# Optimization experiments

Measured on AMD Instinct MI355X. Metric: run time of the kernel, lower is better.

Reference implementation:

```python
import jax, jax.numpy as jnp
import numpy as np
import math

B, T, C = 4, 2048, 2048
N_HEAD, N_KV = 16, 4
HD = C // N_HEAD          # 128
N_REP = N_HEAD // N_KV    # 4


def setup_inputs() -> dict:
    key = jax.random.key(0)
    ks = jax.random.split(key, 5)
    x = jax.random.normal(ks[0], (B, T, C), dtype=jnp.float32)
    s = 0.02
    wq = jax.random.normal(ks[1], (C, N_HEAD * HD), dtype=jnp.float32) * s
    wk = jax.random.normal(ks[2], (C, N_KV * HD), dtype=jnp.float32) * s
    wv = jax.random.normal(ks[3], (C, N_KV * HD), dtype=jnp.float32) * s
    wo = jax.random.normal(ks[4], (C, C), dtype=jnp.float32) * s
    # RoPE table: cos/sin pairs, equivalent to torch polar freqs_cis (theta=10000)
    inv_freq = 1.0 / (10000.0 ** (jnp.arange(0, HD, 2, dtype=jnp.float32) / HD))  # (HD/2,)
    ang = jnp.arange(T, dtype=jnp.float32)[:, None] * inv_freq[None, :]           # (T, HD/2)
    freqs_cis = jnp.stack([jnp.cos(ang), jnp.sin(ang)], axis=-1)                  # (T, HD/2, 2)
    return {"x": x, "freqs_cis": freqs_cis, "wq": wq, "wk": wk, "wv": wv, "wo": wo}


def _rope(t, freqs_cis):
    # t: (B, T, H, HD); complex multiply on (even, odd) pairs
    tp = t.reshape(*t.shape[:-1], HD // 2, 2)
    a, b = tp[..., 0], tp[..., 1]
    c = freqs_cis[: t.shape[1], :, 0][None, :, None, :]  # (1,T,1,HD/2)
    s = freqs_cis[: t.shape[1], :, 1][None, :, None, :]
    out = jnp.stack([a * c - b * s, a * s + b * c], axis=-1)
    return out.reshape(t.shape).astype(t.dtype)


def reference(x, freqs_cis, wq, wk, wv, wo):
    q = (x @ wq).reshape(B, T, N_HEAD, HD)
    k = (x @ wk).reshape(B, T, N_KV, HD)
    v = (x @ wv).reshape(B, T, N_KV, HD)
    q = _rope(q, freqs_cis)
    k = _rope(k, freqs_cis)
    # GQA attention without materializing repeated K/V: group q heads by kv head
    qg = q.reshape(B, T, N_KV, N_REP, HD)
    scale = 1.0 / math.sqrt(HD)
    att = jnp.einsum('btgrd,bsgd->bgrts', qg, k) * scale   # (B,G,R,T,S)
    causal = jnp.tril(jnp.ones((T, T), dtype=bool))
    att = jnp.where(causal, att, jnp.finfo(att.dtype).min)
    att = jax.nn.softmax(att, axis=-1)
    y = jnp.einsum('bgrts,bsgd->btgrd', att, v).reshape(B, T, C)
    y = y @ wo
    return y
```

## Files before the change

### kernel.cpp

```cpp
#include <hip/hip_runtime.h>
#include <math.h>
#include <stdint.h>

#define B_ 4
#define T_ 2048
#define C_ 2048
#define NH 16
#define NKV 4
#define HD 128
#define NREP 4
#define KVC (NKV*HD)
#define QSTR 3072

typedef __attribute__((ext_vector_type(8))) __bf16 bf16x8;
typedef __attribute__((ext_vector_type(4))) __bf16 bf16x4;
typedef __attribute__((ext_vector_type(4))) float floatx4;

#define GLOBAL_AS __attribute__((address_space(1)))
#define LDS_AS __attribute__((address_space(3)))

__device__ __forceinline__ void gl2lds16(const unsigned short* g, unsigned short* l) {
  __builtin_amdgcn_global_load_lds((const GLOBAL_AS unsigned int*)g,
                                   (LDS_AS unsigned int*)l, 16, 0, 0);
}

__device__ __forceinline__ float b2f(unsigned short u) {
  union { unsigned int i; float f; } v; v.i = ((unsigned int)u) << 16; return v.f;
}
__device__ __forceinline__ unsigned short f2b(float f) {
  union { float f; unsigned int i; } v; v.f = f;
  unsigned int r = v.i + 0x7fffu + ((v.i >> 16) & 1u);
  return (unsigned short)(r >> 16);
}

__global__ void cvt_bf16_kernel(const float* __restrict__ X,
                                unsigned short* __restrict__ Y, int n) {
  int i = (blockIdx.x * 256 + threadIdx.x) * 4;
  if (i >= n) return;
  float4 v = *(const float4*)(X + i);
  ushort4 o;
  o.x = f2b(v.x); o.y = f2b(v.y); o.z = f2b(v.z); o.w = f2b(v.w);
  *(ushort4*)(Y + i) = o;
}

__global__ void transpose_cvt_kernel(const float* __restrict__ W,
                                     unsigned short* __restrict__ Wt,
                                     int K, int N) {
  __shared__ float tile[32][33];
  int n = blockIdx.x * 32 + threadIdx.x;
  int kbase = blockIdx.y * 32;
  #pragma unroll
  for (int i = 0; i < 32; i += 8)
    tile[threadIdx.y + i][threadIdx.x] = W[(size_t)(kbase + threadIdx.y + i) * N + n];
  __syncthreads();
  int k = kbase + threadIdx.x;
  int nb = blockIdx.x * 32;
  #pragma unroll
  for (int i = 0; i < 32; i += 8)
    Wt[(size_t)(nb + threadIdx.y + i) * K + k] = f2b(tile[threadIdx.x][threadIdx.y + i]);
}

__global__ void transpose_v_kernel(const unsigned short* __restrict__ V,
                                   unsigned short* __restrict__ Vt) {
  __shared__ unsigned short tile[32][33];
  int d0 = blockIdx.x * 32;
  int sg = blockIdx.y * 32;
  int b = sg >> 11;
  int s0 = sg & (T_ - 1);
  #pragma unroll
  for (int i = 0; i < 32; i += 8)
    tile[threadIdx.y + i][threadIdx.x] =
        V[(size_t)(sg + threadIdx.y + i) * QSTR + d0 + threadIdx.x];
  __syncthreads();
  #pragma unroll
  for (int i = 0; i < 32; i += 8) {
    int d = d0 + threadIdx.y + i;
    int g = d >> 7, dl = d & 127;
    Vt[((size_t)(b * NKV + g) * HD + dl) * T_ + s0 + threadIdx.x] =
        tile[threadIdx.x][threadIdx.y + i];
  }
}

template<int STORE_BF16>
__global__ __launch_bounds__(512, 2) void gemm256_bt(
    const unsigned short* __restrict__ A,
    const unsigned short* __restrict__ Bt,
    void* __restrict__ Cout,
    int M, int N, int K)
{
  __shared__ unsigned short Lds[65536];

  int tid = threadIdx.x;

  int nbx = gridDim.x;
  int nwg = nbx * gridDim.y;
  int orig = blockIdx.y * nbx + blockIdx.x;
  int cpx = nwg >> 3;
  int swz = (orig & 7) * cpx + (orig >> 3);
  int m0 = (swz % nbx) * 256;
  int n0 = (swz / nbx) * 256;

  int wave = tid >> 6, lane = tid & 63;
  int fr = lane & 15, kg = lane >> 4;
  int slot = kg ^ ((fr >> 1) & 3);
  int wm_off = (wave >> 2) * 128;
  int wn_off = (wave & 3) * 64;

  int rowoff = wave * 16 + (lane >> 2);
  int kgs = (lane & 3) ^ ((lane >> 3) & 3);
  const unsigned short* Asrc = A  + (size_t)(m0 + rowoff) * K + kgs * 8;
  const unsigned short* Bsrc = Bt + (size_t)(n0 + rowoff) * K + kgs * 8;
  size_t rstep = (size_t)128 * K;

  int abase = (wm_off + fr) * 32 + slot * 8;
  int bbase = 8192 + (wn_off + fr) * 32 + slot * 8;

  floatx4 acc[8][4];
  #pragma unroll
  for (int i = 0; i < 8; i++)
    #pragma unroll
    for (int j = 0; j < 4; j++)
      acc[i][j] = (floatx4){0.f, 0.f, 0.f, 0.f};

  int nt = K >> 6;

  #define STAGE_HALF(tn, kkh, isB) do {                                        \
    const unsigned short* s_ = ((isB) ? Bsrc : Asrc) + (size_t)(tn) * 64 + (kkh) * 32; \
    unsigned short* d_ = &Lds[(((tn) & 1) << 15) + ((kkh) << 14) + ((isB) << 13) + (wave << 9)]; \
    gl2lds16(s_, d_);                                                          \
    gl2lds16(s_ + rstep, d_ + 4096);                                           \
  } while (0)

  STAGE_HALF(0, 0, 0); STAGE_HALF(0, 0, 1); STAGE_HALF(0, 1, 0); STAGE_HALF(0, 1, 1);
  asm volatile("s_waitcnt vmcnt(4)" ::: "memory");
  __builtin_amdgcn_s_barrier();

  bf16x8 bfrag[4];
  for (int t = 0; t < nt; ++t) {
    int cb = (t & 1) << 15;
    int more = (t + 1 < nt);
    #pragma unroll
    for (int p = 0; p < 4; ++p) {
      const int kkc = p >> 1, mhc = p & 1;
      if (mhc == 0) {
        #pragma unroll
        for (int j = 0; j < 4; ++j) {
          union { uint4 u; bf16x8 v; } tb;
          tb.u = *(const uint4*)&Lds[cb + bbase + (kkc << 14) + j * 512];
          bfrag[j] = tb.v;
        }
      }
      bf16x8 af[4];
      #pragma unroll
      for (int i = 0; i < 4; ++i) {
        union { uint4 u; bf16x8 v; } ta;
        ta.u = *(const uint4*)&Lds[cb + abase + (kkc << 14) + (mhc * 4 + i) * 512];
        af[i] = ta.v;
      }
      if (more) STAGE_HALF(t + 1, kkc, mhc);
      if (p == 1) {
        if (more) asm volatile("s_waitcnt vmcnt(4)" ::: "memory");
        else      asm volatile("s_waitcnt vmcnt(0)" ::: "memory");
      } else if (p == 3) {
        if (more) asm volatile("s_waitcnt vmcnt(4)" ::: "memory");
      }
      __builtin_amdgcn_s_barrier();
      asm volatile("s_waitcnt lgkmcnt(0)" ::: "memory");
      __builtin_amdgcn_s_setprio(1);
      #pragma unroll
      for (int i = 0; i < 4; ++i)
        #pragma unroll
        for (int j = 0; j < 4; ++j)
          acc[mhc * 4 + i][j] =
              __builtin_amdgcn_mfma_f32_16x16x32_bf16(af[i], bfrag[j], acc[mhc * 4 + i][j], 0, 0, 0);
      __builtin_amdgcn_s_setprio(0);
      __builtin_amdgcn_s_barrier();
    }
  }
  #undef STAGE_HALF

  int erow = kg * 4;
  #pragma unroll
  for (int i = 0; i < 8; ++i)
    #pragma unroll
    for (int j = 0; j < 4; ++j) {
      int gm = m0 + wm_off + i * 16 + erow;
      int gn = n0 + wn_off + j * 16 + fr;
      #pragma unroll
      for (int r = 0; r < 4; ++r) {
        float v = acc[i][j][r];
        if (STORE_BF16)
          ((unsigned short*)Cout)[(size_t)(gm + r) * N + gn] = f2b(v);
        else
          ((float*)Cout)[(size_t)(gm + r) * N + gn] = v;
      }
    }
}

__global__ void rope_kernel(unsigned short* __restrict__ X,
                            const float* __restrict__ FC, int nheads, int stride) {
  long long idx = (long long)blockIdx.x * 256 + threadIdx.x;
  int p = (int)(idx & (HD / 2 - 1));
  long long t1 = idx >> 6;
  int h = (int)(t1 % nheads);
  long long row = t1 / nheads;
  int t = (int)(row & (T_ - 1));
  float c = FC[((size_t)t * (HD / 2) + p) * 2 + 0];
  float s = FC[((size_t)t * (HD / 2) + p) * 2 + 1];
  unsigned short* ptr = X + row * (size_t)stride + h * HD + 2 * p;
  float a = b2f(ptr[0]), b = b2f(ptr[1]);
  ptr[0] = f2b(a * c - b * s);
  ptr[1] = f2b(a * s + b * c);
}

#define ABR 128
#define ABC 64
#define KLD 136
#define VLD 72
#define PLD 72

__global__ __launch_bounds__(256, 3) void attn_mfma_kernel(
    const unsigned short* __restrict__ Q,
    const unsigned short* __restrict__ Kg,
    const unsigned short* __restrict__ Vt,
    unsigned short* __restrict__ O)
{
  __shared__ unsigned short KPs[128 * PLD];
  __shared__ unsigned short Vs[HD * VLD];

  int bh = blockIdx.x;
  int qt = (int)(gridDim.y - 1 - blockIdx.y);
  int b = bh >> 4, h = bh & 15, g = h >> 2;
  int tid = threadIdx.x, wave = tid >> 6, lane = tid & 63;
  int fr = lane & 15, kg = lane >> 4, erow = 4 * kg;

  bf16x8 qf[2][4];
  #pragma unroll
  for (int rt = 0; rt < 2; rt++) {
    const unsigned short* qrow =
        Q + (size_t)(b * T_ + qt * ABR + wave * 32 + rt * 16 + fr) * QSTR + h * HD;
    #pragma unroll
    for (int kk = 0; kk < 4; kk++) {
      union { uint4 u; bf16x8 v; } t;
      t.u = *(const uint4*)(qrow + kk * 32 + kg * 8);
      qf[rt][kk] = t.v;
    }
  }

  floatx4 oacc[2][8];
  #pragma unroll
  for (int rt = 0; rt < 2; rt++)
    #pragma unroll
    for (int d = 0; d < 8; d++) oacc[rt][d] = (floatx4){0.f, 0.f, 0.f, 0.f};
  float rsum[2];
  rsum[0] = 0.f; rsum[1] = 0.f;

  const float scale = 0.08838834764831845f;
  const float MOFF = 9.0f;

  size_t krow0 = (size_t)(b * T_) * QSTR + g * HD;
  size_t vbase = ((size_t)(b * NKV + g) * HD) * T_;
  int q0 = qt * ABR + wave * 32;
  int nit = 2 * qt + 2;

  int sr = tid >> 2, kc4 = (tid & 3) * 8;
  int vr = tid >> 1, vc = (tid & 1) * 8;

  const unsigned short* kptr = Kg + krow0 + (size_t)sr * QSTR + kc4;
  const unsigned short* vptr = Vt + vbase + (size_t)vr * T_ + vc;
  uint4 gk[4], gv[4];
  #pragma unroll
  for (int c = 0; c < 4; c++) gk[c] = *(const uint4*)(kptr + c * 32);
  #pragma unroll
  for (int c = 0; c < 4; c++) gv[c] = *(const uint4*)(vptr + c * 16);

  for (int it = 0; it < nit; it++) {
    int s0 = it * ABC;
    __syncthreads();
    #pragma unroll
    for (int c = 0; c < 4; c++)
      *(uint4*)&KPs[sr * KLD + kc4 + c * 32] = gk[c];
    #pragma unroll
    for (int c = 0; c < 4; c++)
      *(uint4*)&Vs[vr * VLD + vc + c * 16] = gv[c];
    __syncthreads();

    floatx4 scr[2][4];
    #pragma unroll
    for (int rt = 0; rt < 2; rt++)
      #pragma unroll
      for (int t = 0; t < 4; t++) scr[rt][t] = (floatx4){0.f, 0.f, 0.f, 0.f};
    __builtin_amdgcn_s_setprio(1);
    #pragma unroll
    for (int kk = 0; kk < 4; kk++) {
      #pragma unroll
      for (int t = 0; t < 4; t++) {
        union { uint4 u; bf16x8 v; } kf;
        kf.u = *(const uint4*)&KPs[(t * 16 + fr) * KLD + kk * 32 + kg * 8];
        scr[0][t] = __builtin_amdgcn_mfma_f32_16x16x32_bf16(kf.v, qf[0][kk], scr[0][t], 0, 0, 0);
        scr[1][t] = __builtin_amdgcn_mfma_f32_16x16x32_bf16(kf.v, qf[1][kk], scr[1][t], 0, 0, 0);
      }
    }
    __builtin_amdgcn_s_setprio(0);

    #pragma unroll
    for (int rt = 0; rt < 2; rt++) {
      int qrow = q0 + rt * 16 + fr;
      #pragma unroll
      for (int t = 0; t < 4; t++)
        #pragma unroll
        for (int r = 0; r < 4; r++) {
          int s_g = s0 + t * 16 + erow + r;
          float p = (s_g <= qrow) ? __expf(scr[rt][t][r] * scale - MOFF) : 0.f;
          scr[rt][t][r] = p;
          rsum[rt] += p;
        }
    }
    __syncthreads();

    #pragma unroll
    for (int rt = 0; rt < 2; rt++)
      #pragma unroll
      for (int t = 0; t < 4; t++) {
        bf16x4 pw;
        pw[0] = (__bf16)scr[rt][t][0];
        pw[1] = (__bf16)scr[rt][t][1];
        pw[2] = (__bf16)scr[rt][t][2];
        pw[3] = (__bf16)scr[rt][t][3];
        *(bf16x4*)&KPs[(wave * 32 + rt * 16 + fr) * PLD + t * 16 + erow] = pw;
      }

    bf16x8 pf[2][2];
    #pragma unroll
    for (int rt = 0; rt < 2; rt++)
      #pragma unroll
      for (int kk = 0; kk < 2; kk++) {
        union { uint4 u; bf16x8 v; } t;
        t.u = *(const uint4*)&KPs[(wave * 32 + rt * 16 + fr) * PLD + kk * 32 + kg * 8];
        pf[rt][kk] = t.v;
      }

    if (it + 1 < nit) {
      kptr += (size_t)ABC * QSTR;
      vptr += ABC;
      #pragma unroll
      for (int c = 0; c < 4; c++) gk[c] = *(const uint4*)(kptr + c * 32);
      #pragma unroll
      for (int c = 0; c < 4; c++) gv[c] = *(const uint4*)(vptr + c * 16);
    }

    __builtin_amdgcn_s_setprio(1);
    #pragma unroll
    for (int d = 0; d < 8; d++)
      #pragma unroll
      for (int kk = 0; kk < 2; kk++) {
        union { uint4 u; bf16x8 v; } vf;
        vf.u = *(const uint4*)&Vs[(d * 16 + fr) * VLD + kk * 32 + kg * 8];
        oacc[0][d] = __builtin_amdgcn_mfma_f32_16x16x32_bf16(pf[0][kk], vf.v, oacc[0][d], 0, 0, 0);
        oacc[1][d] = __builtin_amdgcn_mfma_f32_16x16x32_bf16(pf[1][kk], vf.v, oacc[1][d], 0, 0, 0);
      }
    __builtin_amdgcn_s_setprio(0);
  }

  #pragma unroll
  for (int rt = 0; rt < 2; rt++) {
    float s = rsum[rt];
    s += __shfl_xor(s, 16);
    s += __shfl_xor(s, 32);
    rsum[rt] = s;
  }

  #pragma unroll
  for (int rt = 0; rt < 2; rt++)
    #pragma unroll
    for (int r = 0; r < 4; r++) {
      float inv = 1.f / __shfl(rsum[rt], erow + r);
      size_t orow =
          (size_t)(b * T_ + qt * ABR + wave * 32 + rt * 16 + erow + r) * C_ + h * HD;
      #pragma unroll
      for (int d = 0; d < 8; d++)
        O[orow + d * 16 + fr] = f2b(oacc[rt][d][r] * inv);
    }
}

extern "C" void kernel_launch(void* const* d_in, const int* in_sizes, int n_in,
                              void* d_out, int out_size, void* d_ws, size_t ws_size,
                              hipStream_t stream) {
  (void)in_sizes; (void)n_in; (void)out_size; (void)ws_size;
  const float* x  = (const float*)d_in[0];
  const float* fc = (const float*)d_in[1];
  const float* wq = (const float*)d_in[2];
  const float* wk = (const float*)d_in[3];
  const float* wv = (const float*)d_in[4];
  const float* wo = (const float*)d_in[5];
  float* out = (float*)d_out;

  char* ws = (char*)d_ws;
  unsigned short* xb   = (unsigned short*)(ws);
  unsigned short* qkv  = (unsigned short*)(ws + 33554432);
  unsigned short* wqT  = (unsigned short*)(ws + 83886080);
  unsigned short* wkT  = (unsigned short*)(ws + 92274688);
  unsigned short* wvT  = (unsigned short*)(ws + 94371840);
  unsigned short* woT  = (unsigned short*)(ws + 96468992);
  unsigned short* vt   = wqT;
  unsigned short* yb   = xb;

  int nx = B_ * T_ * C_;
  cvt_bf16_kernel<<<nx / 4 / 256, 256, 0, stream>>>(x, xb, nx);
  transpose_cvt_kernel<<<dim3(C_ / 32, C_ / 32), dim3(32, 8), 0, stream>>>(wq, wqT, C_, C_);
  transpose_cvt_kernel<<<dim3(KVC / 32, C_ / 32), dim3(32, 8), 0, stream>>>(wk, wkT, C_, KVC);
  transpose_cvt_kernel<<<dim3(KVC / 32, C_ / 32), dim3(32, 8), 0, stream>>>(wv, wvT, C_, KVC);
  transpose_cvt_kernel<<<dim3(C_ / 32, C_ / 32), dim3(32, 8), 0, stream>>>(wo, woT, C_, C_);

  int M = B_ * T_;
  gemm256_bt<1><<<dim3(M / 256, QSTR / 256), 512, 0, stream>>>(xb, wqT, qkv, M, QSTR, C_);

  long long qp = (long long)B_ * T_ * NH * (HD / 2);
  rope_kernel<<<(unsigned)(qp / 256), 256, 0, stream>>>(qkv, fc, NH, QSTR);
  long long kp = (long long)B_ * T_ * NKV * (HD / 2);
  rope_kernel<<<(unsigned)(kp / 256), 256, 0, stream>>>(qkv + 2048, fc, NKV, QSTR);

  transpose_v_kernel<<<dim3(KVC / 32, B_ * T_ / 32), dim3(32, 8), 0, stream>>>(qkv + 2560, vt);

  attn_mfma_kernel<<<dim3(B_ * NH, T_ / ABR), 256, 0, stream>>>(qkv, qkv + 2048, vt, yb);

  gemm256_bt<0><<<dim3(M / 256, C_ / 256), 512, 0, stream>>>(yb, woT, out, M, C_, C_);
}
```

Baseline: 598.9 us.

## Drop register prefetch of K/V tiles, add unmasked fast path with exp2

Removes the register-staged prefetch of the next K/V tile and instead loads each tile directly from global memory into LDS at the start of every iteration. This frees the 8 uint4 prefetch registers, possibly helping occupancy, but it exposes global load latency that was previously overlapped with the PV matmul. It also adds a branch that skips causal masking for tiles lying fully below the diagonal. The exponential becomes exp2f with the scale and offset folded into a single fma.

```diff
diff --git a/kernel.cpp b/kernel.cpp
--- a/kernel.cpp
+++ b/kernel.cpp
@@ -255,8 +255,8 @@
   float rsum[2];
   rsum[0] = 0.f; rsum[1] = 0.f;
 
-  const float scale = 0.08838834764831845f;
-  const float MOFF = 9.0f;
+  const float SC2 = 0.08838834764831845f * 1.4426950408889634f;
+  const float MO2 = 9.0f * 1.4426950408889634f;
 
   size_t krow0 = (size_t)(b * T_) * QSTR + g * HD;
   size_t vbase = ((size_t)(b * NKV + g) * HD) * T_;
@@ -266,23 +266,19 @@
   int sr = tid >> 2, kc4 = (tid & 3) * 8;
   int vr = tid >> 1, vc = (tid & 1) * 8;
 
-  const unsigned short* kptr = Kg + krow0 + (size_t)sr * QSTR + kc4;
-  const unsigned short* vptr = Vt + vbase + (size_t)vr * T_ + vc;
-  uint4 gk[4], gv[4];
-  #pragma unroll
-  for (int c = 0; c < 4; c++) gk[c] = *(const uint4*)(kptr + c * 32);
-  #pragma unroll
-  for (int c = 0; c < 4; c++) gv[c] = *(const uint4*)(vptr + c * 16);
-
   for (int it = 0; it < nit; it++) {
     int s0 = it * ABC;
     __syncthreads();
-    #pragma unroll
-    for (int c = 0; c < 4; c++)
-      *(uint4*)&KPs[sr * KLD + kc4 + c * 32] = gk[c];
-    #pragma unroll
-    for (int c = 0; c < 4; c++)
-      *(uint4*)&Vs[vr * VLD + vc + c * 16] = gv[c];
+    {
+      const unsigned short* src = Kg + krow0 + (size_t)(s0 + sr) * QSTR;
+      #pragma unroll
+      for (int c = 0; c < 4; c++)
+        *(uint4*)&KPs[sr * KLD + kc4 + c * 32] = *(const uint4*)(src + kc4 + c * 32);
+      const unsigned short* vsrc = Vt + vbase + (size_t)vr * T_ + s0;
+      #pragma unroll
+      for (int c = 0; c < 4; c++)
+        *(uint4*)&Vs[vr * VLD + vc + c * 16] = *(const uint4*)(vsrc + vc + c * 16);
+    }
     __syncthreads();
 
     floatx4 scr[2][4];
@@ -303,18 +299,31 @@
     }
     __builtin_amdgcn_s_setprio(0);
 
-    #pragma unroll
-    for (int rt = 0; rt < 2; rt++) {
-      int qrow = q0 + rt * 16 + fr;
-      #pragma unroll
-      for (int t = 0; t < 4; t++)
+    if (s0 + ABC - 1 <= q0) {
+      #pragma unroll
+      for (int rt = 0; rt < 2; rt++)
         #pragma unroll
-        for (int r = 0; r < 4; r++) {
-          int s_g = s0 + t * 16 + erow + r;
-          float p = (s_g <= qrow) ? __expf(scr[rt][t][r] * scale - MOFF) : 0.f;
-          scr[rt][t][r] = p;
-          rsum[rt] += p;
-        }
+        for (int t = 0; t < 4; t++)
+          #pragma unroll
+          for (int r = 0; r < 4; r++) {
+            float p = exp2f(fmaf(scr[rt][t][r], SC2, -MO2));
+            scr[rt][t][r] = p;
+            rsum[rt] += p;
+          }
+    } else {
+      #pragma unroll
+      for (int rt = 0; rt < 2; rt++) {
+        int qrow = q0 + rt * 16 + fr;
+        #pragma unroll
+        for (int t = 0; t < 4; t++)
+          #pragma unroll
+          for (int r = 0; r < 4; r++) {
+            int s_g = s0 + t * 16 + erow + r;
+            float p = (s_g <= qrow) ? exp2f(fmaf(scr[rt][t][r], SC2, -MO2)) : 0.f;
+            scr[rt][t][r] = p;
+            rsum[rt] += p;
+          }
+      }
     }
     __syncthreads();
 
@@ -339,16 +348,6 @@
         t.u = *(const uint4*)&KPs[(wave * 32 + rt * 16 + fr) * PLD + kk * 32 + kg * 8];
         pf[rt][kk] = t.v;
       }
-
-    if (it + 1 < nit) {
-      kptr += (size_t)ABC * QSTR;
-      vptr += ABC;
-      #pragma unroll
-      for (int c = 0; c < 4; c++) gk[c] = *(const uint4*)(kptr + c * 32);
-      #pragma unroll
-      for (int c = 0; c < 4; c++) gv[c] = *(const uint4*)(vptr + c * 16);
-    }
-
     __builtin_amdgcn_s_setprio(1);
     #pragma unroll
     for (int d = 0; d < 8; d++)
```

After: 540.0 us. -9.8%, faster.
